# Kernel tuning notes

Hardware: AMD Instinct MI355X
Metric: run time of the kernel (lower is better)

The kernel has to match this reference:

```python
import jax, jax.numpy as jnp
import numpy as np

S, B, H = 2048, 32, 1024

def setup_inputs() -> dict:
    key = jax.random.key(0)
    k1, k2, k3, k4 = jax.random.split(key, 4)
    scale = 1.0 / np.sqrt(H)
    return {
        "rnn_outputs": jax.random.normal(k1, (1, B, H), dtype=jnp.float32),
        "encoder_outputs": jax.random.normal(k2, (S, B, H), dtype=jnp.float32),
        "W_attn": jax.random.normal(k3, (H, H), dtype=jnp.float32) * scale,
        "b_attn": jax.random.normal(k4, (H,), dtype=jnp.float32) * scale,
    }

def reference(rnn_outputs, encoder_outputs, W_attn, b_attn):
    # Luong 'general' attention, vectorized form of the nested-loop original.
    dec = rnn_outputs[0]  # [b, h]
    # nn.Linear: enc @ W.T + b, applied to every (s, b) position -> [s, b, h]
    proj = jnp.einsum('sbh,kh->sbk', encoder_outputs, W_attn) + b_attn
    # energy[b, i] = dec[b] . proj[i, b]  -> [b, s]
    energies = jnp.einsum('bh,sbh->bs', dec, proj)
    return jax.nn.softmax(energies, axis=-1)
```

## Files before the change

### kernel.cpp

```cpp
#include <hip/hip_runtime.h>


#define SS 2048
#define BB 32
#define HH 1024

typedef float vfloat4 __attribute__((ext_vector_type(4)));

__global__ __launch_bounds__(256) void proj_kernel(const float* __restrict__ dec,
                                                   const float* __restrict__ W,
                                                   float* __restrict__ v) {
    __shared__ float ds[HH];
    __shared__ float part[256];
    const int b  = blockIdx.x >> 3;
    const int hc = blockIdx.x & 7;
    for (int i = threadIdx.x; i < HH; i += 256) ds[i] = dec[b * HH + i];
    __syncthreads();
    const int t  = threadIdx.x;
    const int h  = (hc << 7) + (t & 127);
    const int k0 = (t >> 7) << 9;
    float a0 = 0.f, a1 = 0.f;
    #pragma unroll 8
    for (int k = 0; k < 512; k += 2) {
        a0 = fmaf(ds[k0 + k],     W[(size_t)(k0 + k) * HH + h],     a0);
        a1 = fmaf(ds[k0 + k + 1], W[(size_t)(k0 + k + 1) * HH + h], a1);
    }
    part[t] = a0 + a1;
    __syncthreads();
    if (t < 128) v[b * HH + h] = part[t] + part[t + 128];
}

__global__ __launch_bounds__(256) void energy_kernel(const float* __restrict__ enc,
                                                     const float* __restrict__ v,
                                                     float* __restrict__ e) {
    const int wid  = (blockIdx.x * 256 + threadIdx.x) >> 6;
    const int lane = threadIdx.x & 63;
    const int s = wid >> 5;
    const int b = wid & 31;
    const vfloat4* ep = (const vfloat4*)(enc + ((size_t)s * BB + b) * HH);
    const vfloat4* vp = (const vfloat4*)(v + (size_t)b * HH);
    float sum = 0.f;
    #pragma unroll
    for (int i = 0; i < 4; ++i) {
        vfloat4 x = __builtin_nontemporal_load(&ep[i * 64 + lane]);
        vfloat4 w = vp[i * 64 + lane];
        sum += x.x * w.x + x.y * w.y + x.z * w.z + x.w * w.w;
    }
    #pragma unroll
    for (int off = 32; off > 0; off >>= 1) sum += __shfl_down(sum, off, 64);
    if (lane == 0) e[b * SS + s] = sum;
}

__global__ __launch_bounds__(256) void softmax_kernel(float* __restrict__ e) {
    const int b = blockIdx.x;
    vfloat4* p = (vfloat4*)(e + (size_t)b * SS);
    const int t    = threadIdx.x;
    const int wave = t >> 6;
    const int lane = t & 63;
    __shared__ float red[4];

    vfloat4 x0 = p[t];
    vfloat4 x1 = p[t + 256];

    float m = fmaxf(fmaxf(fmaxf(x0.x, x0.y), fmaxf(x0.z, x0.w)),
                    fmaxf(fmaxf(x1.x, x1.y), fmaxf(x1.z, x1.w)));
    #pragma unroll
    for (int off = 32; off > 0; off >>= 1) m = fmaxf(m, __shfl_down(m, off, 64));
    if (lane == 0) red[wave] = m;
    __syncthreads();
    m = fmaxf(fmaxf(red[0], red[1]), fmaxf(red[2], red[3]));
    __syncthreads();

    x0.x = __expf(x0.x - m); x0.y = __expf(x0.y - m);
    x0.z = __expf(x0.z - m); x0.w = __expf(x0.w - m);
    x1.x = __expf(x1.x - m); x1.y = __expf(x1.y - m);
    x1.z = __expf(x1.z - m); x1.w = __expf(x1.w - m);

    float s = (x0.x + x0.y + x0.z + x0.w) + (x1.x + x1.y + x1.z + x1.w);
    #pragma unroll
    for (int off = 32; off > 0; off >>= 1) s += __shfl_down(s, off, 64);
    if (lane == 0) red[wave] = s;
    __syncthreads();
    const float inv = 1.0f / (red[0] + red[1] + red[2] + red[3]);

    x0 *= inv;
    x1 *= inv;
    p[t]       = x0;
    p[t + 256] = x1;
}

extern "C" void kernel_launch(void* const* d_in, const int* in_sizes, int n_in,
                              void* d_out, int out_size, void* d_ws, size_t ws_size,
                              hipStream_t stream) {
    const float* rnn = (const float*)d_in[0];
    const float* enc = (const float*)d_in[1];
    const float* W   = (const float*)d_in[2];
    float* out = (float*)d_out;
    float* v   = (float*)d_ws;

    proj_kernel<<<BB * 8, 256, 0, stream>>>(rnn, W, v);
    energy_kernel<<<(SS * BB) / 4, 256, 0, stream>>>(enc, v, out);
    softmax_kernel<<<BB, 256, 0, stream>>>(out);
}
```

Baseline: 363.8 us.

## Vectorize projection GEMV with finer k-split and more blocks; split energy accumulators

The projection kernel now assigns each thread four output columns via float4 loads of W and splits the reduction dimension into 16 groups of 64. This shortens each thread's serial FMA chain and doubles the block count, with partial sums reduced through shared memory. The energy kernel uses two independent accumulators and drops the nontemporal load hint on the encoder stream, which could change cache behavior for the large streaming read.

New measurement: 368.6 us. About the same (+1.3%).

```diff
diff --git a/kernel.cpp b/kernel.cpp
--- a/kernel.cpp
+++ b/kernel.cpp
@@ -11,23 +11,30 @@
                                                    const float* __restrict__ W,
                                                    float* __restrict__ v) {
     __shared__ float ds[HH];
-    __shared__ float part[256];
-    const int b  = blockIdx.x >> 3;
-    const int hc = blockIdx.x & 7;
+    __shared__ float part[16 * 64];
+    const int b  = blockIdx.x >> 4;
+    const int hc = blockIdx.x & 15;
     for (int i = threadIdx.x; i < HH; i += 256) ds[i] = dec[b * HH + i];
     __syncthreads();
-    const int t  = threadIdx.x;
-    const int h  = (hc << 7) + (t & 127);
-    const int k0 = (t >> 7) << 9;
-    float a0 = 0.f, a1 = 0.f;
+    const int t   = threadIdx.x;
+    const int ht  = t & 15;
+    const int kg  = t >> 4;
+    const int col = (hc << 4) + ht;
+    const int kbase = kg << 6;
+    const vfloat4* __restrict__ Wp = (const vfloat4*)W;
+    vfloat4 acc = {0.f, 0.f, 0.f, 0.f};
     #pragma unroll 8
-    for (int k = 0; k < 512; k += 2) {
-        a0 = fmaf(ds[k0 + k],     W[(size_t)(k0 + k) * HH + h],     a0);
-        a1 = fmaf(ds[k0 + k + 1], W[(size_t)(k0 + k + 1) * HH + h], a1);
+    for (int k = 0; k < 64; ++k) {
+        acc += ds[kbase + k] * Wp[(size_t)(kbase + k) * (HH / 4) + col];
     }
-    part[t] = a0 + a1;
+    ((vfloat4*)part)[(kg << 4) + ht] = acc;
     __syncthreads();
-    if (t < 128) v[b * HH + h] = part[t] + part[t + 128];
+    if (t < 64) {
+        float s = 0.f;
+        #pragma unroll
+        for (int g = 0; g < 16; ++g) s += part[(g << 6) + t];
+        v[b * HH + (hc << 6) + t] = s;
+    }
 }
 
 __global__ __launch_bounds__(256) void energy_kernel(const float* __restrict__ enc,
@@ -37,15 +44,19 @@
     const int lane = threadIdx.x & 63;
     const int s = wid >> 5;
     const int b = wid & 31;
-    const vfloat4* ep = (const vfloat4*)(enc + ((size_t)s * BB + b) * HH);
-    const vfloat4* vp = (const vfloat4*)(v + (size_t)b * HH);
-    float sum = 0.f;
+    const vfloat4* __restrict__ ep = (const vfloat4*)(enc + ((size_t)s * BB + b) * HH);
+    const vfloat4* __restrict__ vp = (const vfloat4*)(v + (size_t)b * HH);
+    float a0 = 0.f, a1 = 0.f;
     #pragma unroll
-    for (int i = 0; i < 4; ++i) {
-        vfloat4 x = __builtin_nontemporal_load(&ep[i * 64 + lane]);
-        vfloat4 w = vp[i * 64 + lane];
-        sum += x.x * w.x + x.y * w.y + x.z * w.z + x.w * w.w;
+    for (int i = 0; i < 4; i += 2) {
+        vfloat4 x0 = ep[(i    ) * 64 + lane];
+        vfloat4 x1 = ep[(i + 1) * 64 + lane];
+        vfloat4 w0 = vp[(i    ) * 64 + lane];
+        vfloat4 w1 = vp[(i + 1) * 64 + lane];
+        a0 += x0.x * w0.x + x0.y * w0.y + x0.z * w0.z + x0.w * w0.w;
+        a1 += x1.x * w1.x + x1.y * w1.y + x1.z * w1.z + x1.w * w1.w;
     }
+    float sum = a0 + a1;
     #pragma unroll
     for (int off = 32; off > 0; off >>= 1) sum += __shfl_down(sum, off, 64);
     if (lane == 0) e[b * SS + s] = sum;
@@ -98,7 +109,7 @@
     float* out = (float*)d_out;
     float* v   = (float*)d_ws;
 
-    proj_kernel<<<BB * 8, 256, 0, stream>>>(rnn, W, v);
+    proj_kernel<<<BB * 16, 256, 0, stream>>>(rnn, W, v);
     energy_kernel<<<(SS * BB) / 4, 256, 0, stream>>>(enc, v, out);
     softmax_kernel<<<BB, 256, 0, stream>>>(out);
 }
```
